# Kernel tuning notes

Measured on AMD Instinct MI355X. Metric: run time of the kernel, lower is better.

Reference implementation:

```python
import jax, jax.numpy as jnp
import numpy as np

D, R, C = 4, 6, 32
P = 2 * R + 1          # 13 (both pixel patch and memory patch, since memory_patch_R == R)
N = P * P              # 169
DIL_INT = 15


def corr_sampler(f1, f2, p, dil):
    """SpatialCorrelationSampler(kernel_size=1, patch_size=p, dilation_patch=dil).
    out[b,i,j,y,x] = sum_c f1[b,c,y,x] * f2[b,c, y+(i-Rp)*dil, x+(j-Rp)*dil] (zero pad)."""
    Rp = (p - 1) // 2
    pad = Rp * dil
    b, c, h, w = f1.shape
    f2p = jnp.pad(f2, ((0, 0), (0, 0), (pad, pad), (pad, pad)))
    outs = [jnp.einsum('bchw,bchw->bhw', f1, f2p[:, :, i * dil:i * dil + h, j * dil:j * dil + w])
            for i in range(p) for j in range(p)]
    return jnp.stack(outs, 1).reshape(b, p, p, h, w)


def bilinear_gather(im, ys, xs):
    """Bilinear sample im [b,c,H,W] at float coords ys,xs [b,N,h,w]; zeros outside."""
    H, W = im.shape[2], im.shape[3]
    y0 = jnp.floor(ys)
    x0 = jnp.floor(xs)
    wy = ys - y0
    wx = xs - x0

    def g(yi, xi):
        valid = ((yi >= 0) & (yi < H) & (xi >= 0) & (xi < W)).astype(im.dtype)
        yc = jnp.clip(yi, 0, H - 1).astype(jnp.int32)
        xc = jnp.clip(xi, 0, W - 1).astype(jnp.int32)
        out = jax.vmap(lambda imb, yb, xb: imb[:, yb, xb])(im, yc, xc)  # [b,c,N,h,w]
        return out * valid[:, None]

    return (g(y0, x0) * ((1 - wy) * (1 - wx))[:, None]
            + g(y0, x0 + 1) * ((1 - wy) * wx)[:, None]
            + g(y0 + 1, x0) * (wy * (1 - wx))[:, None]
            + g(y0 + 1, x0 + 1) * (wy * wx)[:, None])


def deform_im2col(im, offset, p):
    """Deformable im2col: for each output pixel (y,x) and kernel pos (ky,kx),
    bilinearly sample im at (y+ky-Rp+off_y, x+kx-Rp+off_x). offset [...,0]=x, [...,1]=y.
    Returns [b,c,p*p,h,w]."""
    b, c, h, w = im.shape
    Rp = (p - 1) // 2
    ky, kx = jnp.meshgrid(jnp.arange(p) - Rp, jnp.arange(p) - Rp, indexing='ij')
    ky = ky.reshape(-1).astype(im.dtype)
    kx = kx.reshape(-1).astype(im.dtype)
    ys = (jnp.arange(h, dtype=im.dtype)[None, None, :, None]
          + ky[None, :, None, None] + offset[..., 1][:, None])  # [b,N,h,w]
    xs = (jnp.arange(w, dtype=im.dtype)[None, None, None, :]
          + kx[None, :, None, None] + offset[..., 0][:, None])
    return bilinear_gather(im, ys, xs)


def unfold_patches(x, p, pad):
    """F.unfold(kernel_size=p, padding=pad) -> [b,c,p*p,h,w]."""
    b, c, h, w = x.shape
    xp = jnp.pad(x, ((0, 0), (0, 0), (pad, pad), (pad, pad)))
    cols = [xp[:, :, i:i + h, j:j + w] for i in range(p) for j in range(p)]
    return jnp.stack(cols, 2)


def _forward(feats_r, feats_t, quantized_r, ref_index, current_ind):
    ri = np.asarray(ref_index)
    ci = int(current_ind)
    diffs = [ci - int(x) for x in ri]
    nsearch = sum(1 for d in diffs if d > DIL_INT)
    dirates = [min(4, d // DIL_INT + 1) for d in diffs if d > DIL_INT]
    nref = feats_r.shape[0]
    b, c, h, w = feats_t.shape

    # offset grid: _y,_x = meshgrid(ij) so grid[...,0]=x-offset, grid[...,1]=y-offset
    _y, _x = jnp.meshgrid(jnp.arange(-R, R + 1), jnp.arange(-R, R + 1), indexing='ij')
    grid = jnp.stack([_x, _y], -1).astype(feats_t.dtype)  # [P,P,2]

    corrs_pixel = []
    offset0 = []
    for s in range(nsearch):
        cc = corr_sampler(feats_t, feats_r[s], P, dirates[s])             # [b,P,P,h,w]
        soft = jax.nn.softmax(cc.reshape(b, N, h * w), axis=1).reshape(b, P, P, h, w)
        off = jnp.einsum('bijhw,ijd->bhwd', soft, grid) * dirates[s]      # [b,h,w,2]
        offset0.append(off)
        col0 = deform_im2col(feats_r[s], off, P)                          # [b,c,N,h,w]
        corrs_pixel.append(jnp.einsum('bchw,bcnhw->bnhw', feats_t, col0).reshape(b, N, h * w))
    for ind in range(nsearch, nref):
        corrs_pixel.append(corr_sampler(feats_t, feats_r[ind], P, 1).reshape(b, N, h * w))

    corr_pixel = jax.nn.softmax(jnp.concatenate(corrs_pixel, 1), axis=1)  # [b,nref*N,h*w]

    # prep: float + stride-D subsampling (C-channel input, so no one-hot branch)
    qr = [quantized_r[i][:, :, ::D, ::D] for i in range(nref)]            # [b,C,h,w]
    cols = [deform_im2col(qr[i], offset0[i], P).reshape(b, C, N, h * w) for i in range(nsearch)]
    cols += [unfold_patches(qr[i], P, R).reshape(b, C, N, h * w) for i in range(nsearch, nref)]
    image_uf = jnp.concatenate(cols, 2)                                   # [b,C,nref*N,h*w]

    out = jnp.einsum('bkl,bckl->bcl', corr_pixel, image_uf).reshape(b, C, h, w)
    return out


def setup_inputs() -> dict:
    key = jax.random.key(0)
    k1, k2, k3 = jax.random.split(key, 3)
    feats_r = jax.random.normal(k1, (3, 1, 64, 56, 56), jnp.float32) * 0.2
    feats_t = jax.random.normal(k2, (1, 64, 56, 56), jnp.float32) * 0.2
    quantized_r = jax.random.uniform(k3, (3, 1, 32, 224, 224), jnp.float32)
    return {
        'feats_r': feats_r,
        'feats_t': feats_t,
        'quantized_r': quantized_r,
        'ref_index': np.array([0, 30, 39], dtype=np.int64),
        'current_ind': 40,
    }


def reference(feats_r, feats_t, quantized_r, ref_index, current_ind):
    return _forward(feats_r, feats_t, quantized_r, ref_index, current_ind)
```

## Files before the change

### kernel.cpp

```cpp
#include <hip/hip_runtime.h>

#define HW    56
#define NPIX  3136
#define CH    64
#define CQ    32
#define PS    13
#define NPOS  169
#define GS    14
#define NG    196
#define G1    15
#define NG1   225

typedef __attribute__((ext_vector_type(8))) short short8;
typedef __attribute__((ext_vector_type(4))) float f32x4;

__device__ inline ushort f2bf(float f) {
  unsigned u = __float_as_uint(f);
  return (ushort)((u + 0x7fffu + ((u >> 16) & 1u)) >> 16);
}
__device__ inline float bf2f(ushort u) {
  return __uint_as_float((unsigned)u << 16);
}
__device__ inline void wave_sync() {
  asm volatile("s_waitcnt lgkmcnt(0)" ::: "memory");
  __builtin_amdgcn_sched_barrier(0);
}

__global__ __launch_bounds__(256) void prep_all(
    const float* __restrict__ ft_in,
    const float* __restrict__ fr_in,
    const float* __restrict__ q_in,
    ushort* __restrict__ ft_out,
    ushort* __restrict__ fr_out,
    ushort* __restrict__ qout,
    float* __restrict__ zrow) {
  __shared__ float smem[CQ * (HW + 1)];
  int bid = blockIdx.x, tid = threadIdx.x;
  if (bid < 784) {
    if (bid == 0 && tid < 64) zrow[tid] = 0.f;
    int m = bid / 196, t = bid - m * 196;
    int row0 = (t / 98) * 32;
    int col0 = (t - (t / 98) * 98) * 32;
    const float* src = (m == 0) ? ft_in : fr_in + (size_t)(m - 1) * CH * NPIX;
    ushort* dst      = (m == 0) ? ft_out : fr_out + (size_t)(m - 1) * NPIX * CH;
    int tx = tid & 31, ty = tid >> 5;
    for (int r = ty; r < 32; r += 8)
      smem[r * 33 + tx] = src[(size_t)(row0 + r) * NPIX + col0 + tx];
    __syncthreads();
    for (int r = ty; r < 32; r += 8)
      dst[(size_t)(col0 + r) * CH + row0 + tx] = f2bf(smem[tx * 33 + r]);
  } else {
    int q = bid - 784;
    int r = q / HW, yy = q - r * HW;
    for (int idx = tid; idx < CQ * HW; idx += 256) {
      int c = idx / HW, xx = idx - c * HW;
      smem[c * (HW + 1) + xx] = q_in[((size_t)(r * CQ + c) * 224 + yy * 4) * 224 + xx * 4];
    }
    __syncthreads();
    for (int idx = tid; idx < CQ * HW; idx += 256) {
      int xx = idx >> 5, c = idx & 31;
      qout[(size_t)r * NPIX * CQ + (size_t)(yy * HW + xx) * CQ + c] = f2bf(smem[c * (HW + 1) + xx]);
    }
  }
}

__global__ __launch_bounds__(256, 4) void colorizer_main(
    const ushort* __restrict__ ftb,
    const ushort* __restrict__ frb,
    const ushort* __restrict__ qrb,
    const ushort* __restrict__ zrow,
    float* __restrict__ out)
{
  __shared__ float C1[1024];
  __shared__ float C2[1024];
  __shared__ int   pw[4 * 832];
  __shared__ float m2s[4], Sas[4];
  __shared__ float fqr0[128];
  __shared__ float red2[512];

  int tid = threadIdx.x;
  int wid = tid >> 6, lane = tid & 63;
  int mrow = lane & 15, klane = lane >> 4;

  int bx = blockIdx.x % 28, by = blockIdx.x / 28;
  int Y0 = by * 2, X0 = bx * 2;
  int dy = wid >> 1, dx = wid & 1;
  int y = Y0 + dy, x = X0 + dx;
  int pix = y * HW + x;

  int*   wb   = pw + wid * 832;
  float* e    = (float*)wb;
  float* D    = (float*)(wb + 176);
  float* wg   = (float*)(wb + 384);
  int*   offg = wb + 608;
  float* cc   = (float*)offg;

  if (lane < 16) offg[208 + lane] = -1;

  const ushort* frb0 = frb;
  const ushort* frb1 = frb + (size_t)NPIX * CH;
  const ushort* frb2 = frb + (size_t)2 * NPIX * CH;
  const ushort* qr0b = qrb;
  const ushort* qr1b = qrb + (size_t)NPIX * CQ;
  const ushort* qr2b = qrb + (size_t)2 * NPIX * CQ;

  const ushort* fb = ftb + (size_t)pix * CH;
  const ushort* plo = (mrow == 0) ? (fb + klane * 8) : zrow;
  const ushort* phi = (mrow == 0) ? (fb + 32 + klane * 8) : zrow;
  short8 b_lo = *(const short8*)plo;
  short8 b_hi = *(const short8*)phi;

  const ushort* fb4 = (mrow < 4)
      ? (ftb + (size_t)((Y0 + (mrow >> 1)) * HW + X0 + (mrow & 1)) * CH)
      : zrow;
  short8 b4_lo = *(const short8*)(fb4 + klane * 8);
  short8 b4_hi = *(const short8*)(fb4 + 32 + klane * 8);

#pragma unroll
  for (int k = 0; k < 8; ++k) {
    int j = wid + 4 * k;
    if (j < 30) {
      int r = (j >= 15);
      int t = j - r * 15;
      int g = t * 16 + mrow;
      int gy = g / G1, gx = g - gy * G1;
      int sy = Y0 - 6 + gy, sx = X0 - 6 + gx;
      bool v = (g < NG1) && ((unsigned)sy < HW) && ((unsigned)sx < HW);
      const ushort* base = r ? frb2 : frb1;
      const ushort* rb = v ? (base + (size_t)(sy * HW + sx) * CH) : zrow;
      short8 alo = *(const short8*)(rb + klane * 8);
      short8 ahi = *(const short8*)(rb + 32 + klane * 8);
      f32x4 acc = {0.f, 0.f, 0.f, 0.f};
      acc = __builtin_amdgcn_mfma_f32_16x16x32_bf16(alo, b4_lo, acc, 0, 0, 0);
      acc = __builtin_amdgcn_mfma_f32_16x16x32_bf16(ahi, b4_hi, acc, 0, 0, 0);
      int col = lane & 15;
      if (col < 4) {
        float* Cd = r ? C2 : C1;
        int row0 = t * 16 + (lane >> 4) * 4;
#pragma unroll
        for (int q = 0; q < 4; ++q) Cd[(row0 + q) * 4 + col] = acc[q];
      }
    }
  }
  __syncthreads();

#pragma unroll
  for (int g = 0; g < 11; ++g) {
    int d = g * 16 + mrow;
    int ii = d / PS, jj = d - ii * PS;
    int sy = y + (ii - 6) * 3, sx = x + (jj - 6) * 3;
    bool v = (d < NPOS) && ((unsigned)sy < HW) && ((unsigned)sx < HW);
    const ushort* rb = v ? (frb0 + (size_t)(sy * HW + sx) * CH) : zrow;
    short8 alo = *(const short8*)(rb + klane * 8);
    short8 ahi = *(const short8*)(rb + 32 + klane * 8);
    f32x4 acc = {0.f, 0.f, 0.f, 0.f};
    acc = __builtin_amdgcn_mfma_f32_16x16x32_bf16(alo, b_lo, acc, 0, 0, 0);
    acc = __builtin_amdgcn_mfma_f32_16x16x32_bf16(ahi, b_hi, acc, 0, 0, 0);
    if (mrow == 0) *(f32x4*)&cc[g * 16 + klane * 4] = acc;
  }
  wave_sync();

  float vs[3];
  float mx = -1e30f;
#pragma unroll
  for (int k = 0; k < 3; ++k) {
    int id = lane + 64 * k;
    float c = (id < NPOS) ? cc[id] : -1e30f;
    vs[k] = c;
    mx = fmaxf(mx, c);
  }
#pragma unroll
  for (int o = 1; o < 64; o <<= 1) mx = fmaxf(mx, __shfl_xor(mx, o));
  float se = 0.f, sxe = 0.f, sye = 0.f;
#pragma unroll
  for (int k = 0; k < 3; ++k) {
    int id = lane + 64 * k;
    if (id < NPOS) {
      float ex = __expf(vs[k] - mx);
      int pi = id / PS, pj = id - pi * PS;
      se += ex;
      sxe += ex * (float)(pj - 6);
      sye += ex * (float)(pi - 6);
    }
  }
#pragma unroll
  for (int o = 1; o < 64; o <<= 1) {
    se  += __shfl_xor(se, o);
    sxe += __shfl_xor(sxe, o);
    sye += __shfl_xor(sye, o);
  }
  float offx = 3.f * sxe / se;
  float offy = 3.f * sye / se;

  float fy0 = floorf(offy), fx0 = floorf(offx);
  int   iy0 = (int)fy0,     ix0 = (int)fx0;
  float wyf = offy - fy0,   wxf = offx - fx0;
  float w00 = (1.f - wyf) * (1.f - wxf), w01 = (1.f - wyf) * wxf;
  float w10 = wyf * (1.f - wxf),         w11 = wyf * wxf;

#pragma unroll
  for (int g = 0; g < 13; ++g) {
    int d = g * 16 + mrow;
    int a = d / GS, bq = d - a * GS;
    int sy = y + iy0 + a - 6, sx = x + ix0 + bq - 6;
    bool vA = (d < NG) && ((unsigned)sy < HW) && ((unsigned)sx < HW);
    int roA = sy * HW + sx;
    const ushort* rbA = vA ? (frb0 + (size_t)roA * CH) : zrow;
    short8 aAlo = *(const short8*)(rbA + klane * 8);
    short8 aAhi = *(const short8*)(rbA + 32 + klane * 8);
    f32x4 accA = {0.f, 0.f, 0.f, 0.f};
    accA = __builtin_amdgcn_mfma_f32_16x16x32_bf16(aAlo, b_lo, accA, 0, 0, 0);
    accA = __builtin_amdgcn_mfma_f32_16x16x32_bf16(aAhi, b_hi, accA, 0, 0, 0);
    if (klane == 0) offg[d] = vA ? roA : -1;
    if (mrow == 0) *(f32x4*)&D[g * 16 + klane * 4] = accA;
  }
  wave_sync();

#pragma unroll
  for (int k = 0; k < 3; ++k) {
    int id = lane + 64 * k;
    if (id < NPOS) {
      int pi = id / PS, pj = id - (id / PS) * PS;
      e[id] = w00 * D[pi * GS + pj]       + w01 * D[pi * GS + pj + 1]
            + w10 * D[(pi + 1) * GS + pj] + w11 * D[(pi + 1) * GS + pj + 1];
    } else if (id < 176) {
      e[id] = -1e30f;
    }
  }
  wave_sync();

  float mx2 = -1e30f;
#pragma unroll
  for (int k = 0; k < 3; ++k) {
    int id = lane + 64 * k;
    if (id < 176) mx2 = fmaxf(mx2, e[id]);
    if (id < NPOS) {
      int ii = id / PS, jj = id - (id / PS) * PS;
      int g = (ii + dy) * G1 + (jj + dx);
      mx2 = fmaxf(mx2, fmaxf(C1[g * 4 + wid], C2[g * 4 + wid]));
    }
  }
#pragma unroll
  for (int o = 1; o < 64; o <<= 1) mx2 = fmaxf(mx2, __shfl_xor(mx2, o));
  float ps = 0.f;
#pragma unroll
  for (int k = 0; k < 3; ++k) {
    int id = lane + 64 * k;
    if (id < 176) {
      float ex = __expf(e[id] - mx2);
      e[id] = ex;
      ps += ex;
    }
    if (id < NPOS) {
      int ii = id / PS, jj = id - (id / PS) * PS;
      int g = (ii + dy) * G1 + (jj + dx);
      ps += __expf(C1[g * 4 + wid] - mx2) + __expf(C2[g * 4 + wid] - mx2);
    }
  }
#pragma unroll
  for (int o = 1; o < 64; o <<= 1) ps += __shfl_xor(ps, o);
  if (lane == 0) { m2s[wid] = mx2; Sas[wid] = ps; }
  wave_sync();

#pragma unroll
  for (int k = 0; k < 4; ++k) {
    int t = lane + 64 * k;
    if (t < 224) {
      float acc = 0.f;
      if (t < NG) {
        int a = t / GS, b = t - (t / GS) * GS;
        if (a < PS && b < PS) acc += w00 * e[a * PS + b];
        if (a < PS && b >= 1) acc += w01 * e[a * PS + b - 1];
        if (a >= 1 && b < PS) acc += w10 * e[(a - 1) * PS + b];
        if (a >= 1 && b >= 1) acc += w11 * e[(a - 1) * PS + b - 1];
      }
      wg[t] = acc;
    }
  }
  wave_sync();

  int slot = lane >> 3, ln = lane & 7;
  f32x4 acc0 = {0.f, 0.f, 0.f, 0.f};
#pragma unroll
  for (int k = 0; k < 28; ++k) {
    int d = slot + k * 8;
    int ro = offg[d];
    if (ro >= 0) {
      float w = wg[d];
      ushort4 u = *(const ushort4*)(qr0b + (size_t)ro * CQ + ln * 4);
      acc0.x = fmaf(w, bf2f(u.x), acc0.x);
      acc0.y = fmaf(w, bf2f(u.y), acc0.y);
      acc0.z = fmaf(w, bf2f(u.z), acc0.z);
      acc0.w = fmaf(w, bf2f(u.w), acc0.w);
    }
  }
#pragma unroll
  for (int o = 8; o <= 32; o <<= 1) {
    acc0.x += __shfl_xor(acc0.x, o);
    acc0.y += __shfl_xor(acc0.y, o);
    acc0.z += __shfl_xor(acc0.z, o);
    acc0.w += __shfl_xor(acc0.w, o);
  }
  if (lane < 8) {
    fqr0[wid * 32 + lane * 4 + 0] = acc0.x;
    fqr0[wid * 32 + lane * 4 + 1] = acc0.y;
    fqr0[wid * 32 + lane * 4 + 2] = acc0.z;
    fqr0[wid * 32 + lane * 4 + 3] = acc0.w;
  }
  __syncthreads();

#pragma unroll
  for (int t = 0; t < 8; ++t) {
    int idx = tid + t * 256;
    int ref = idx >> 10;
    int ix = idx & 1023;
    int g = ix >> 2, p = ix & 3;
    int gy = g / G1, gx = g - gy * G1;
    int ii = gy - (p >> 1), jj = gx - (p & 1);
    bool win = (g < NG1) && ((unsigned)ii < PS) && ((unsigned)jj < PS);
    float* Cd = ref ? C2 : C1;
    float val = Cd[ix];
    Cd[ix] = win ? __expf(val - m2s[p]) : 0.f;
  }
  __syncthreads();

  int q8 = tid & 7, s = tid >> 3;
  float a12[4][4];
#pragma unroll
  for (int p = 0; p < 4; ++p)
#pragma unroll
    for (int c = 0; c < 4; ++c) a12[p][c] = 0.f;
#pragma unroll
  for (int i = 0; i < 8; ++i) {
    int g = s + 32 * i;
    if (g < NG1) {
      int gy = g / G1, gx = g - gy * G1;
      int sy = Y0 - 6 + gy, sx = X0 - 6 + gx;
      if (((unsigned)sy < HW) && ((unsigned)sx < HW)) {
        size_t ro = (size_t)(sy * HW + sx) * CQ + q8 * 4;
        ushort4 u1 = *(const ushort4*)(qr1b + ro);
        ushort4 u2 = *(const ushort4*)(qr2b + ro);
        f32x4 w1 = *(f32x4*)&C1[g * 4];
        f32x4 w2 = *(f32x4*)&C2[g * 4];
        float q1[4] = {bf2f(u1.x), bf2f(u1.y), bf2f(u1.z), bf2f(u1.w)};
        float q2[4] = {bf2f(u2.x), bf2f(u2.y), bf2f(u2.z), bf2f(u2.w)};
#pragma unroll
        for (int p = 0; p < 4; ++p)
#pragma unroll
          for (int c = 0; c < 4; ++c)
            a12[p][c] += w1[p] * q1[c] + w2[p] * q2[c];
      }
    }
  }
#pragma unroll
  for (int o = 8; o <= 32; o <<= 1)
#pragma unroll
    for (int p = 0; p < 4; ++p)
#pragma unroll
      for (int c = 0; c < 4; ++c)
        a12[p][c] += __shfl_xor(a12[p][c], o);
  if (lane < 8) {
#pragma unroll
    for (int p = 0; p < 4; ++p)
#pragma unroll
      for (int c = 0; c < 4; ++c)
        red2[wid * 128 + lane * 16 + p * 4 + c] = a12[p][c];
  }
  __syncthreads();

  if (tid < 128) {
    int p = tid >> 5, c = tid & 31;
    float tot = fqr0[p * 32 + c];
#pragma unroll
    for (int w = 0; w < 4; ++w)
      tot += red2[w * 128 + (c >> 2) * 16 + p * 4 + (c & 3)];
    int pidx = (Y0 + (p >> 1)) * HW + X0 + (p & 1);
    out[(size_t)c * NPIX + pidx] = tot / Sas[p];
  }
}

extern "C" void kernel_launch(void* const* d_in, const int* in_sizes, int n_in,
                              void* d_out, int out_size, void* d_ws, size_t ws_size,
                              hipStream_t stream) {
  const float* feats_r     = (const float*)d_in[0];
  const float* feats_t     = (const float*)d_in[1];
  const float* quantized_r = (const float*)d_in[2];

  ushort* ftb = (ushort*)d_ws;
  ushort* frb = ftb + 200704;
  ushort* qrb = frb + 602112;
  float*  zro = (float*)(qrb + 301056);

  prep_all<<<952, 256, 0, stream>>>(feats_t, feats_r, quantized_r,
                                    ftb, frb, qrb, zro);
  colorizer_main<<<784, 256, 0, stream>>>(ftb, frb, qrb, (const ushort*)zro,
                                          (float*)d_out);
}
```

Before: 45.80 us.

## Drop softmax max-subtraction, vectorize prep transpose and reference-0 gather loads

Removes the max-reduction passes before both softmaxes and exponentiates the raw correlation scores directly. This saves a wave-wide shuffle reduction and an extra LDS pass, relying on the inputs being small enough not to overflow exp. The prep transpose now uses float4 loads and ushort4 stores. The reference-0 gather uses 16-byte ushort8 loads with 16 slots instead of 8, which halves the loop trips but adds more shuffle work.

New measurement: 44.13 us. 1.04x faster.

```diff
diff --git a/kernel.cpp b/kernel.cpp
--- a/kernel.cpp
+++ b/kernel.cpp
@@ -12,6 +12,7 @@
 #define NG1   225
 
 typedef __attribute__((ext_vector_type(8))) short short8;
+typedef __attribute__((ext_vector_type(8))) ushort ushort8;
 typedef __attribute__((ext_vector_type(4))) float f32x4;
 
 __device__ inline ushort f2bf(float f) {
@@ -43,12 +44,17 @@
     int col0 = (t - (t / 98) * 98) * 32;
     const float* src = (m == 0) ? ft_in : fr_in + (size_t)(m - 1) * CH * NPIX;
     ushort* dst      = (m == 0) ? ft_out : fr_out + (size_t)(m - 1) * NPIX * CH;
-    int tx = tid & 31, ty = tid >> 5;
-    for (int r = ty; r < 32; r += 8)
-      smem[r * 33 + tx] = src[(size_t)(row0 + r) * NPIX + col0 + tx];
+    int ty = tid >> 3, tx4 = (tid & 7) * 4;
+    f32x4 v = *(const f32x4*)&src[(size_t)(row0 + ty) * NPIX + col0 + tx4];
+    *(f32x4*)&smem[ty * 33 + tx4] = v;
     __syncthreads();
-    for (int r = ty; r < 32; r += 8)
-      dst[(size_t)(col0 + r) * CH + row0 + tx] = f2bf(smem[tx * 33 + r]);
+    int px = tid >> 3, c4 = (tid & 7) * 4;
+    ushort4 o;
+    o.x = f2bf(smem[(c4 + 0) * 33 + px]);
+    o.y = f2bf(smem[(c4 + 1) * 33 + px]);
+    o.z = f2bf(smem[(c4 + 2) * 33 + px]);
+    o.w = f2bf(smem[(c4 + 3) * 33 + px]);
+    *(ushort4*)&dst[(size_t)(col0 + px) * CH + row0 + c4] = o;
   } else {
     int q = bid - 784;
     int r = q / HW, yy = q - r * HW;
@@ -74,7 +80,7 @@
   __shared__ float C1[1024];
   __shared__ float C2[1024];
   __shared__ int   pw[4 * 832];
-  __shared__ float m2s[4], Sas[4];
+  __shared__ float Sas[4];
   __shared__ float fqr0[128];
   __shared__ float red2[512];
 
@@ -160,24 +166,13 @@
   }
   wave_sync();
 
-  float vs[3];
-  float mx = -1e30f;
-#pragma unroll
-  for (int k = 0; k < 3; ++k) {
-    int id = lane + 64 * k;
-    float c = (id < NPOS) ? cc[id] : -1e30f;
-    vs[k] = c;
-    mx = fmaxf(mx, c);
-  }
-#pragma unroll
-  for (int o = 1; o < 64; o <<= 1) mx = fmaxf(mx, __shfl_xor(mx, o));
   float se = 0.f, sxe = 0.f, sye = 0.f;
 #pragma unroll
   for (int k = 0; k < 3; ++k) {
     int id = lane + 64 * k;
     if (id < NPOS) {
-      float ex = __expf(vs[k] - mx);
-      int pi = id / PS, pj = id - pi * PS;
+      float ex = __expf(cc[id]);
+      int pi = id / PS, pj = id - (id / PS) * PS;
       se += ex;
       sxe += ex * (float)(pj - 6);
       sye += ex * (float)(pi - 6);
@@ -216,50 +211,29 @@
   }
   wave_sync();
 
+  float ps = 0.f;
 #pragma unroll
   for (int k = 0; k < 3; ++k) {
     int id = lane + 64 * k;
     if (id < NPOS) {
       int pi = id / PS, pj = id - (id / PS) * PS;
-      e[id] = w00 * D[pi * GS + pj]       + w01 * D[pi * GS + pj + 1]
-            + w10 * D[(pi + 1) * GS + pj] + w11 * D[(pi + 1) * GS + pj + 1];
+      float c0 = w00 * D[pi * GS + pj]       + w01 * D[pi * GS + pj + 1]
+               + w10 * D[(pi + 1) * GS + pj] + w11 * D[(pi + 1) * GS + pj + 1];
+      float ex = __expf(c0);
+      e[id] = ex;
+      ps += ex;
     } else if (id < 176) {
-      e[id] = -1e30f;
-    }
-  }
-  wave_sync();
-
-  float mx2 = -1e30f;
-#pragma unroll
-  for (int k = 0; k < 3; ++k) {
-    int id = lane + 64 * k;
-    if (id < 176) mx2 = fmaxf(mx2, e[id]);
+      e[id] = 0.f;
+    }
     if (id < NPOS) {
       int ii = id / PS, jj = id - (id / PS) * PS;
       int g = (ii + dy) * G1 + (jj + dx);
-      mx2 = fmaxf(mx2, fmaxf(C1[g * 4 + wid], C2[g * 4 + wid]));
-    }
-  }
-#pragma unroll
-  for (int o = 1; o < 64; o <<= 1) mx2 = fmaxf(mx2, __shfl_xor(mx2, o));
-  float ps = 0.f;
-#pragma unroll
-  for (int k = 0; k < 3; ++k) {
-    int id = lane + 64 * k;
-    if (id < 176) {
-      float ex = __expf(e[id] - mx2);
-      e[id] = ex;
-      ps += ex;
-    }
-    if (id < NPOS) {
-      int ii = id / PS, jj = id - (id / PS) * PS;
-      int g = (ii + dy) * G1 + (jj + dx);
-      ps += __expf(C1[g * 4 + wid] - mx2) + __expf(C2[g * 4 + wid] - mx2);
+      ps += __expf(C1[g * 4 + wid]) + __expf(C2[g * 4 + wid]);
     }
   }
 #pragma unroll
   for (int o = 1; o < 64; o <<= 1) ps += __shfl_xor(ps, o);
-  if (lane == 0) { m2s[wid] = mx2; Sas[wid] = ps; }
+  if (lane == 0) Sas[wid] = ps;
   wave_sync();
 
 #pragma unroll
@@ -268,44 +242,39 @@
     if (t < 224) {
       float acc = 0.f;
       if (t < NG) {
-        int a = t / GS, b = t - (t / GS) * GS;
-        if (a < PS && b < PS) acc += w00 * e[a * PS + b];
-        if (a < PS && b >= 1) acc += w01 * e[a * PS + b - 1];
-        if (a >= 1 && b < PS) acc += w10 * e[(a - 1) * PS + b];
-        if (a >= 1 && b >= 1) acc += w11 * e[(a - 1) * PS + b - 1];
+        int a = t / GS, bq2 = t - (t / GS) * GS;
+        if (a < PS && bq2 < PS) acc += w00 * e[a * PS + bq2];
+        if (a < PS && bq2 >= 1) acc += w01 * e[a * PS + bq2 - 1];
+        if (a >= 1 && bq2 < PS) acc += w10 * e[(a - 1) * PS + bq2];
+        if (a >= 1 && bq2 >= 1) acc += w11 * e[(a - 1) * PS + bq2 - 1];
       }
       wg[t] = acc;
     }
   }
   wave_sync();
 
-  int slot = lane >> 3, ln = lane & 7;
-  f32x4 acc0 = {0.f, 0.f, 0.f, 0.f};
-#pragma unroll
-  for (int k = 0; k < 28; ++k) {
-    int d = slot + k * 8;
+  int slot = lane >> 2, ln4 = lane & 3;
+  float acc8[8];
+#pragma unroll
+  for (int c = 0; c < 8; ++c) acc8[c] = 0.f;
+#pragma unroll
+  for (int k = 0; k < 14; ++k) {
+    int d = slot + k * 16;
     int ro = offg[d];
     if (ro >= 0) {
       float w = wg[d];
-      ushort4 u = *(const ushort4*)(qr0b + (size_t)ro * CQ + ln * 4);
-      acc0.x = fmaf(w, bf2f(u.x), acc0.x);
-      acc0.y = fmaf(w, bf2f(u.y), acc0.y);
-      acc0.z = fmaf(w, bf2f(u.z), acc0.z);
-      acc0.w = fmaf(w, bf2f(u.w), acc0.w);
-    }
-  }
-#pragma unroll
-  for (int o = 8; o <= 32; o <<= 1) {
-    acc0.x += __shfl_xor(acc0.x, o);
-    acc0.y += __shfl_xor(acc0.y, o);
-    acc0.z += __shfl_xor(acc0.z, o);
-    acc0.w += __shfl_xor(acc0.w, o);
-  }
-  if (lane < 8) {
-    fqr0[wid * 32 + lane * 4 + 0] = acc0.x;
-    fqr0[wid * 32 + lane * 4 + 1] = acc0.y;
-    fqr0[wid * 32 + lane * 4 + 2] = acc0.z;
-    fqr0[wid * 32 + lane * 4 + 3] = acc0.w;
+      ushort8 u = *(const ushort8*)(qr0b + (size_t)ro * CQ + ln4 * 8);
+#pragma unroll
+      for (int c = 0; c < 8; ++c) acc8[c] = fmaf(w, bf2f(u[c]), acc8[c]);
+    }
+  }
+#pragma unroll
+  for (int o = 4; o <= 32; o <<= 1)
+#pragma unroll
+    for (int c = 0; c < 8; ++c) acc8[c] += __shfl_xor(acc8[c], o);
+  if (lane < 4) {
+#pragma unroll
+    for (int c = 0; c < 8; ++c) fqr0[wid * 32 + lane * 8 + c] = acc8[c];
   }
   __syncthreads();
 
@@ -320,7 +289,7 @@
     bool win = (g < NG1) && ((unsigned)ii < PS) && ((unsigned)jj < PS);
     float* Cd = ref ? C2 : C1;
     float val = Cd[ix];
-    Cd[ix] = win ? __expf(val - m2s[p]) : 0.f;
+    Cd[ix] = win ? __expf(val) : 0.f;
   }
   __syncthreads();
 
```
